# Kernel tuning notes

Measured on AMD Instinct MI355X. Metric: run time of the kernel, lower is better.

The kernel has to match this reference:

```python
import jax, jax.numpy as jnp
import numpy as np

B, L, D, H = 2, 256, 512, 8
DH = D // H
EPS = 1e-12
NEG = -1000000000000000.0


def setup_inputs() -> dict:
    key = jax.random.key(0)
    ks = jax.random.split(key, 16)
    s = 0.02
    return {
        "inputs": jax.random.normal(ks[0], (B, L, D), jnp.float32),
        "pos_embedding": jax.random.normal(ks[1], (B, L, L, D), jnp.float32),
        "seq_mask": jnp.ones((B, L), jnp.int32),
        "Wq": jax.random.normal(ks[2], (D, D), jnp.float32) * s,
        "bq": jnp.zeros((D,), jnp.float32),
        "Wk": jax.random.normal(ks[3], (D, D), jnp.float32) * s,
        "bk": jnp.zeros((D,), jnp.float32),
        "Wv": jax.random.normal(ks[4], (D, D), jnp.float32) * s,
        "bv": jnp.zeros((D,), jnp.float32),
        "Wr": jax.random.normal(ks[5], (D, D), jnp.float32) * s,
        "br": jnp.zeros((D,), jnp.float32),
        "u": jax.random.normal(ks[6], (H, DH), jnp.float32),
        "v": jax.random.normal(ks[7], (H, DH), jnp.float32),
        "Wf": jax.random.normal(ks[8], (D, D), jnp.float32) * s,
        "bf": jnp.zeros((D,), jnp.float32),
        "gamma": jnp.ones((D,), jnp.float32),
        "beta": jnp.zeros((D,), jnp.float32),
    }


def _layer_norm(x, gamma, beta, eps):
    mu = jnp.mean(x, axis=-1, keepdims=True)
    var = jnp.mean(jnp.square(x - mu), axis=-1, keepdims=True)
    return (x - mu) * jax.lax.rsqrt(var + eps) * gamma + beta


def reference(inputs, pos_embedding, seq_mask, Wq, bq, Wk, bk, Wv, bv, Wr, br,
              u, v, Wf, bf, gamma, beta):
    b, l, d = inputs.shape
    # projections (nn.Linear: x @ W.T + b)
    q = (inputs @ Wq.T + bq).reshape(b, l, H, DH).transpose(0, 2, 1, 3)  # [B,H,L,DH]
    k = (inputs @ Wk.T + bk).reshape(b, l, H, DH).transpose(0, 2, 1, 3)
    vv = (inputs @ Wv.T + bv).reshape(b, l, H, DH).transpose(0, 2, 1, 3)
    rel = (pos_embedding @ Wr.T + br).reshape(b, l, l, H, DH)            # [B,L,L,H,DH]

    # A + C: content-content + content-bias
    A_C = jnp.einsum('bhid,bhjd->bhij', q + u[None, :, None, :], k)
    # B + D: position term against per-(i,j) relative embeddings
    B_D = jnp.einsum('bhid,bijhd->bhij', q + v[None, :, None, :], rel)

    score = (A_C + B_D) / np.sqrt(DH).astype(np.float32)
    invalid = (seq_mask == 0)[:, None, None, :]   # mask keys where seq_mask==0
    score = jnp.where(invalid, NEG, score)
    attn = jax.nn.softmax(score, axis=-1)

    ctx = jnp.einsum('bhij,bhjd->bhid', attn, vv)
    ctx = ctx.transpose(0, 2, 1, 3).reshape(b, l, d)

    # FFN (single dense) + residual + LayerNorm
    h = ctx @ Wf.T + bf
    return _layer_norm(h + inputs, gamma, beta, EPS)
```

## Files before the change

kernel.cpp:

```cpp
#include <hip/hip_runtime.h>
#include <cmath>

typedef __bf16 bf16x8 __attribute__((ext_vector_type(8)));
typedef float f32x4 __attribute__((ext_vector_type(4)));

__device__ __forceinline__ float4 ld4(const float* p) { return *reinterpret_cast<const float4*>(p); }
__device__ __forceinline__ void st4(float* p, float4 v) { *reinterpret_cast<float4*>(p) = v; }
__device__ __forceinline__ void fma4(float4& a, float s, const float4& v) {
    a.x = fmaf(s, v.x, a.x); a.y = fmaf(s, v.y, a.y);
    a.z = fmaf(s, v.z, a.z); a.w = fmaf(s, v.w, a.w);
}
__device__ __forceinline__ float dot4(const float4& a, const float4& b) {
    return a.x*b.x + a.y*b.y + a.z*b.z + a.w*b.w;
}
__device__ __forceinline__ unsigned short f2bf(float f) {
    unsigned int x = __float_as_uint(f);
    unsigned int r = x + 0x7FFFu + ((x >> 16) & 1u);
    return (unsigned short)(r >> 16);
}
__device__ __forceinline__ ushort4 cvt4u(float4 a) {
    ushort4 u;
    u.x = f2bf(a.x); u.y = f2bf(a.y); u.z = f2bf(a.z); u.w = f2bf(a.w);
    return u;
}
__device__ __forceinline__ bf16x8 cvt8(float4 a, float4 b) {
    bf16x8 r;
    r[0] = (__bf16)a.x; r[1] = (__bf16)a.y; r[2] = (__bf16)a.z; r[3] = (__bf16)a.w;
    r[4] = (__bf16)b.x; r[5] = (__bf16)b.y; r[6] = (__bf16)b.z; r[7] = (__bf16)b.w;
    return r;
}

__device__ __forceinline__ void mfma_tile(
        const float* __restrict__ Abase, int ldA,
        const float* __restrict__ Bbase, int ldB,
        int K, int lane, f32x4 acc[4]) {
    int koff = (lane >> 4) * 8;
    int rr = lane & 15;
    const float* ap = Abase + rr * ldA + koff;
    const float* bp = Bbase + rr * ldB + koff;
#pragma unroll 2
    for (int k0 = 0; k0 < K; k0 += 32) {
        float4 a0  = ld4(ap + k0),            a1  = ld4(ap + k0 + 4);
        float4 b00 = ld4(bp + k0),            b01 = ld4(bp + k0 + 4);
        float4 b10 = ld4(bp + 16*ldB + k0),   b11 = ld4(bp + 16*ldB + k0 + 4);
        float4 b20 = ld4(bp + 32*ldB + k0),   b21 = ld4(bp + 32*ldB + k0 + 4);
        float4 b30 = ld4(bp + 48*ldB + k0),   b31 = ld4(bp + 48*ldB + k0 + 4);
        bf16x8 af = cvt8(a0, a1);
        acc[0] = __builtin_amdgcn_mfma_f32_16x16x32_bf16(af, cvt8(b00, b01), acc[0], 0, 0, 0);
        acc[1] = __builtin_amdgcn_mfma_f32_16x16x32_bf16(af, cvt8(b10, b11), acc[1], 0, 0, 0);
        acc[2] = __builtin_amdgcn_mfma_f32_16x16x32_bf16(af, cvt8(b20, b21), acc[2], 0, 0, 0);
        acc[3] = __builtin_amdgcn_mfma_f32_16x16x32_bf16(af, cvt8(b30, b31), acc[3], 0, 0, 0);
    }
}

__global__ __launch_bounds__(256) void k_front(
        const float* __restrict__ x,
        const float* __restrict__ Wq, const float* __restrict__ Wk, const float* __restrict__ Wv,
        const float* __restrict__ bq, const float* __restrict__ bk, const float* __restrict__ bv,
        const float* __restrict__ Wr,
        float* __restrict__ qw, float* __restrict__ kw, float* __restrict__ vw,
        float* __restrict__ wrt) {
    int id = blockIdx.x;
    int t = threadIdx.x;
    if (id < 192) {
        int mat = id >> 6, rem = id & 63;
        int m0 = (rem >> 3) * 64, n0 = (rem & 7) * 64;
        const float* W   = (mat == 0) ? Wq : (mat == 1) ? Wk : Wv;
        const float* bias= (mat == 0) ? bq : (mat == 1) ? bk : bv;
        float* out       = (mat == 0) ? qw : (mat == 1) ? kw : vw;
        int wv = t >> 6, lane = t & 63;
        f32x4 acc[4] = {{0,0,0,0},{0,0,0,0},{0,0,0,0},{0,0,0,0}};
        mfma_tile(x + (m0 + wv * 16) * 512, 512, W + n0 * 512, 512, 512, lane, acc);
        int h = n0 >> 6;
        int col = lane & 15, rbase = (lane >> 4) * 4;
#pragma unroll
        for (int c = 0; c < 4; c++) {
            int d = c * 16 + col;
            float bv_ = bias[n0 + d];
#pragma unroll
            for (int r = 0; r < 4; r++) {
                int m = m0 + wv * 16 + rbase + r;
                int b = m >> 8, i = m & 255;
                out[((b * 8 + h) * 256 + i) * 64 + d] = acc[c][r] + bv_;
            }
        }
    } else {
        __shared__ float tile[64][65];
        int id2 = id - 192;
        int n0 = (id2 >> 3) * 64, k0 = (id2 & 7) * 64;
        int tx = t & 63, ty = t >> 6;
#pragma unroll
        for (int r = 0; r < 16; r++) {
            int row = ty * 16 + r;
            tile[row][tx] = Wr[(n0 + row) * 512 + k0 + tx];
        }
        __syncthreads();
#pragma unroll
        for (int r = 0; r < 16; r++) {
            int row = ty * 16 + r;
            wrt[(k0 + row) * 512 + n0 + tx] = tile[tx][row];
        }
    }
}

__global__ __launch_bounds__(256) void k_mid(
        const float* __restrict__ qw, const float* __restrict__ kw,
        const float* __restrict__ wrt,
        const float* __restrict__ u, const float* __restrict__ vb, const float* __restrict__ br,
        float* __restrict__ w_ws, float* __restrict__ ac_ws) {
    int id = blockIdx.x;
    int t = threadIdx.x, wv = t >> 6, lane = t & 63;
    __shared__ float red[8][64];
    if (id < 512) {
        int h = id >> 6, rem = id & 63;
        int m0 = (rem >> 3) * 64, n0 = (rem & 7) * 64;
        int b = m0 >> 8, i0 = m0 & 255;
        {
            int e = t & 63, grp = t >> 6;
            const float* wr_row = wrt + (size_t)(n0 + e) * 512 + h * 64 + grp * 16;
            const float* vbh = vb + h * 64 + grp * 16;
            float s = 0.f;
#pragma unroll
            for (int d = 0; d < 16; d += 4) s += dot4(ld4(wr_row + d), ld4(vbh + d));
            red[grp][e] = s;
        }
        __syncthreads();
        __shared__ float vwr_l[64];
        if (t < 64) vwr_l[t] = red[0][t] + red[1][t] + red[2][t] + red[3][t];
        f32x4 acc[4] = {{0,0,0,0},{0,0,0,0},{0,0,0,0},{0,0,0,0}};
        mfma_tile(qw + ((b * 8 + h) * 256 + i0 + wv * 16) * 64, 64,
                  wrt + (size_t)n0 * 512 + h * 64, 512, 64, lane, acc);
        __syncthreads();
        int col = lane & 15, rbase = (lane >> 4) * 4;
#pragma unroll
        for (int c = 0; c < 4; c++) {
            float vw_ = vwr_l[c * 16 + col];
            int n = n0 + c * 16 + col;
#pragma unroll
            for (int r = 0; r < 4; r++) {
                int m = m0 + wv * 16 + rbase + r;
                w_ws[((size_t)m * 8 + h) * 512 + n] = acc[c][r] + vw_;
            }
        }
    } else {
        int id2 = id - 512;
        int bh = id2 >> 4, rem2 = id2 & 15;
        int b = bh >> 3, h = bh & 7;
        int i0 = (rem2 >> 2) * 64, j0 = (rem2 & 3) * 64;
        {
            int xx = t & 63, grp = t >> 6;
            const float* qrow = qw + ((b * 8 + h) * 256 + i0 + xx) * 64 + grp * 16;
            const float* brh = br + h * 64 + grp * 16;
            const float* vbh = vb + h * 64 + grp * 16;
            float s = 0.f;
#pragma unroll
            for (int d = 0; d < 16; d += 4) {
                float4 q4 = ld4(qrow + d), b4 = ld4(brh + d), v4 = ld4(vbh + d);
                s += (q4.x + v4.x) * b4.x + (q4.y + v4.y) * b4.y
                   + (q4.z + v4.z) * b4.z + (q4.w + v4.w) * b4.w;
            }
            red[grp][xx] = s;
            const float* krow = kw + ((b * 8 + h) * 256 + j0 + xx) * 64 + grp * 16;
            const float* uh = u + h * 64 + grp * 16;
            s = 0.f;
#pragma unroll
            for (int d = 0; d < 16; d += 4) s += dot4(ld4(krow + d), ld4(uh + d));
            red[4 + grp][xx] = s;
        }
        __syncthreads();
        __shared__ float c_l[64], uk_l[64];
        if (t < 64) c_l[t] = red[0][t] + red[1][t] + red[2][t] + red[3][t];
        else if (t < 128) { int y = t - 64; uk_l[y] = red[4][y] + red[5][y] + red[6][y] + red[7][y]; }
        f32x4 acc[4] = {{0,0,0,0},{0,0,0,0},{0,0,0,0},{0,0,0,0}};
        mfma_tile(qw + ((b * 8 + h) * 256 + i0 + wv * 16) * 64, 64,
                  kw + ((b * 8 + h) * 256 + j0) * 64, 64, 64, lane, acc);
        __syncthreads();
        int col = lane & 15, rbase = (lane >> 4) * 4;
#pragma unroll
        for (int c = 0; c < 4; c++) {
            int j = j0 + c * 16 + col;
            float ukv = uk_l[c * 16 + col];
#pragma unroll
            for (int r = 0; r < 4; r++) {
                int ii = wv * 16 + rbase + r;
                ac_ws[((b * 256 + i0 + ii) * 8 + h) * 256 + j] = acc[c][r] + ukv + c_l[ii];
            }
        }
    }
}

__global__ __launch_bounds__(512, 4) void k_attn(
        const float* __restrict__ pos, const float* __restrict__ w_ws,
        const float* __restrict__ ac_ws, const float* __restrict__ vw,
        const int* __restrict__ seq_mask, float* __restrict__ ctx) {
    int bi = blockIdx.x;
    int b = bi >> 8, i = bi & 255;
    int t = threadIdx.x;
    int wv = t >> 6, lane = t & 63;
    __shared__ unsigned short wl[8 * 512];
    __shared__ float sc[8][256];
    __shared__ unsigned short stage[8][4096];

    {
        int h = t >> 6;
        int e0 = (t & 63) * 8;
        const float* src = w_ws + ((size_t)bi * 8 + h) * 512 + e0;
        float4 a = ld4(src);
        float4 c = ld4(src + 4);
        *reinterpret_cast<ushort4*>(&wl[h * 512 + e0])     = cvt4u(a);
        *reinterpret_cast<ushort4*>(&wl[h * 512 + e0 + 4]) = cvt4u(c);
    }
    __syncthreads();

    const float* pb = pos + (size_t)bi * (256 * 512);
    int jbase = wv * 32;
    unsigned short* sb = &stage[wv][0];
    int arow = lane & 15;
    int koff = (lane >> 4) * 8;

#pragma unroll
    for (int jt = 0; jt < 2; jt++) {
        f32x4 acc = {0, 0, 0, 0};
#pragma unroll
        for (int eh = 0; eh < 2; eh++) {
            const float* src = pb + (size_t)(jbase + jt * 16) * 512 + eh * 256 + lane * 4;
            float4 tmp[16];
#pragma unroll
            for (int s = 0; s < 16; s++) tmp[s] = ld4(src + s * 512);
#pragma unroll
            for (int s = 0; s < 16; s++) {
                *reinterpret_cast<ushort4*>(&sb[s * 256 + lane * 4]) = cvt4u(tmp[s]);
            }
#pragma unroll
            for (int es = 0; es < 8; es++) {
                bf16x8 af = *reinterpret_cast<const bf16x8*>(&sb[arow * 256 + es * 32 + koff]);
                bf16x8 bf = *reinterpret_cast<const bf16x8*>(&wl[(lane & 7) * 512 + (eh * 8 + es) * 32 + koff]);
                acc = __builtin_amdgcn_mfma_f32_16x16x32_bf16(af, bf, acc, 0, 0, 0);
            }
        }
        int h = lane & 15;
        int rbase = (lane >> 4) * 4;
        if (h < 8) {
#pragma unroll
            for (int r = 0; r < 4; r++) sc[h][jbase + jt * 16 + rbase + r] = acc[r];
        }
    }
    __syncthreads();

    {
        int h = wv;
        const float* acrow = ac_ws + ((b * 256 + i) * 8 + h) * 256;
        float vals[4];
        float mx = -INFINITY;
#pragma unroll
        for (int r = 0; r < 4; r++) {
            int j = lane + r * 64;
            float s = (sc[h][j] + acrow[j]) * 0.125f;
            if (seq_mask[b * 256 + j] == 0) s = -1e15f;
            vals[r] = s;
            mx = fmaxf(mx, s);
        }
#pragma unroll
        for (int m = 32; m >= 1; m >>= 1) mx = fmaxf(mx, __shfl_xor(mx, m, 64));
        float sum = 0.f;
#pragma unroll
        for (int r = 0; r < 4; r++) { vals[r] = __expf(vals[r] - mx); sum += vals[r]; }
#pragma unroll
        for (int m = 32; m >= 1; m >>= 1) sum += __shfl_xor(sum, m, 64);
        float inv = 1.0f / sum;
#pragma unroll
        for (int r = 0; r < 4; r++) sc[h][lane + r * 64] = vals[r] * inv;
    }

    float4* part = reinterpret_cast<float4*>(&stage[0][0]);
    {
        int h = wv;
        int d4 = (lane & 15) * 4;
        int js = lane >> 4;
        const float* vbase = vw + (size_t)(b * 8 + h) * 256 * 64 + d4;
        float4 acc = {0, 0, 0, 0};
#pragma unroll 2
        for (int r = 0; r < 64; r += 4) {
            int j = js * 64 + r;
            float p0 = sc[h][j + 0], p1 = sc[h][j + 1];
            float p2 = sc[h][j + 2], p3 = sc[h][j + 3];
            float4 v0 = ld4(vbase + (size_t)(j + 0) * 64);
            float4 v1 = ld4(vbase + (size_t)(j + 1) * 64);
            float4 v2 = ld4(vbase + (size_t)(j + 2) * 64);
            float4 v3 = ld4(vbase + (size_t)(j + 3) * 64);
            fma4(acc, p0, v0); fma4(acc, p1, v1);
            fma4(acc, p2, v2); fma4(acc, p3, v3);
        }
        part[(h * 4 + js) * 16 + (lane & 15)] = acc;
    }
    {
        int h = wv;
        if ((lane >> 4) == 0) {
            int l = lane & 15;
            float4 a0 = part[(h * 4 + 0) * 16 + l], a1 = part[(h * 4 + 1) * 16 + l];
            float4 a2 = part[(h * 4 + 2) * 16 + l], a3 = part[(h * 4 + 3) * 16 + l];
            float4 o;
            o.x = a0.x + a1.x + a2.x + a3.x;
            o.y = a0.y + a1.y + a2.y + a3.y;
            o.z = a0.z + a1.z + a2.z + a3.z;
            o.w = a0.w + a1.w + a2.w + a3.w;
            st4(ctx + (size_t)(b * 256 + i) * 512 + h * 64 + l * 4, o);
        }
    }
}

__global__ __launch_bounds__(256) void k_ffn(
        const float* __restrict__ A, const float* __restrict__ Wf,
        const float* __restrict__ bias, const float* __restrict__ resid,
        float* __restrict__ outp) {
    int m0 = blockIdx.x * 64, n0 = blockIdx.y * 64;
    int t = threadIdx.x, wv = t >> 6, lane = t & 63;
    f32x4 acc[4] = {{0,0,0,0},{0,0,0,0},{0,0,0,0},{0,0,0,0}};
    mfma_tile(A + (m0 + wv * 16) * 512, 512, Wf + n0 * 512, 512, 512, lane, acc);
    int col = lane & 15, rbase = (lane >> 4) * 4;
#pragma unroll
    for (int c = 0; c < 4; c++) {
        int n = n0 + c * 16 + col;
        float bv_ = bias[n];
#pragma unroll
        for (int r = 0; r < 4; r++) {
            int m = m0 + wv * 16 + rbase + r;
            outp[m * 512 + n] = acc[c][r] + bv_ + resid[m * 512 + n];
        }
    }
}

__global__ __launch_bounds__(256) void k_ln(
        const float* __restrict__ tmp, const float* __restrict__ gamma,
        const float* __restrict__ beta, float* __restrict__ out) {
    int m = blockIdx.x, t = threadIdx.x;
    int wv = t >> 6, lane = t & 63;
    float2 xv = *reinterpret_cast<const float2*>(&tmp[m * 512 + t * 2]);
    __shared__ float red[4];
    float s = xv.x + xv.y;
#pragma unroll
    for (int k = 32; k >= 1; k >>= 1) s += __shfl_xor(s, k, 64);
    if (lane == 0) red[wv] = s;
    __syncthreads();
    float mu = (red[0] + red[1] + red[2] + red[3]) * (1.0f / 512.0f);
    __syncthreads();
    float dx = xv.x - mu, dy = xv.y - mu;
    float vs = dx * dx + dy * dy;
#pragma unroll
    for (int k = 32; k >= 1; k >>= 1) vs += __shfl_xor(vs, k, 64);
    if (lane == 0) red[wv] = vs;
    __syncthreads();
    float var = (red[0] + red[1] + red[2] + red[3]) * (1.0f / 512.0f);
    float rstd = rsqrtf(var + 1e-12f);
    float2 g = *reinterpret_cast<const float2*>(&gamma[t * 2]);
    float2 be = *reinterpret_cast<const float2*>(&beta[t * 2]);
    float2 o;
    o.x = dx * rstd * g.x + be.x;
    o.y = dy * rstd * g.y + be.y;
    *reinterpret_cast<float2*>(&out[m * 512 + t * 2]) = o;
}

extern "C" void kernel_launch(void* const* d_in, const int* in_sizes, int n_in,
                              void* d_out, int out_size, void* d_ws, size_t ws_size,
                              hipStream_t stream) {
    const float* x     = (const float*)d_in[0];
    const float* pos   = (const float*)d_in[1];
    const int*   smask = (const int*)d_in[2];
    const float* Wq = (const float*)d_in[3];
    const float* bq = (const float*)d_in[4];
    const float* Wk = (const float*)d_in[5];
    const float* bk = (const float*)d_in[6];
    const float* Wv = (const float*)d_in[7];
    const float* bv = (const float*)d_in[8];
    const float* Wr = (const float*)d_in[9];
    const float* br = (const float*)d_in[10];
    const float* u  = (const float*)d_in[11];
    const float* vb = (const float*)d_in[12];
    const float* Wf = (const float*)d_in[13];
    const float* bf = (const float*)d_in[14];
    const float* gamma = (const float*)d_in[15];
    const float* beta  = (const float*)d_in[16];
    float* out = (float*)d_out;

    float* ws = (float*)d_ws;
    float* q_ws   = ws;
    float* k_ws   = q_ws  + 262144;
    float* v_ws   = k_ws  + 262144;
    float* w_ws   = v_ws  + 262144;
    float* ac_ws  = w_ws  + 2097152;
    float* ctx_ws = ac_ws + 1048576;
    float* tmp_ws = ctx_ws + 262144;
    float* wrt_ws = tmp_ws + 262144;

    k_front<<<dim3(256), 256, 0, stream>>>(x, Wq, Wk, Wv, bq, bk, bv, Wr,
                                           q_ws, k_ws, v_ws, wrt_ws);
    k_mid<<<dim3(768), 256, 0, stream>>>(q_ws, k_ws, wrt_ws, u, vb, br, w_ws, ac_ws);
    k_attn<<<dim3(512), 512, 0, stream>>>(pos, w_ws, ac_ws, v_ws, smask, ctx_ws);
    k_ffn<<<dim3(8, 8), 256, 0, stream>>>(ctx_ws, Wf, bf, x, tmp_ws);
    k_ln<<<dim3(512), 256, 0, stream>>>(tmp_ws, gamma, beta, out);
}
```

Before: 110.7 us.

## Fuse FFN GEMM with residual add and LayerNorm into one kernel

Merges the output projection GEMM and the LayerNorm into a single kernel. Each block computes 16 full rows of 512 columns, so row statistics can be reduced in registers and shared memory, and the intermediate tmp buffer write and re-read go away. This also removes one kernel launch. In exchange the grid shrinks from 64 blocks to 32, each doing more serial work with B loaded directly from global memory. Variance now uses the single-pass E[x^2]-mu^2 form, which is slightly less numerically robust.

```diff
diff --git a/kernel.cpp b/kernel.cpp
--- a/kernel.cpp
+++ b/kernel.cpp
@@ -1,5 +1,6 @@
 #include <hip/hip_runtime.h>
 #include <cmath>
+
 
 typedef __bf16 bf16x8 __attribute__((ext_vector_type(8)));
 typedef float f32x4 __attribute__((ext_vector_type(4)));
@@ -309,55 +310,84 @@
     }
 }
 
-__global__ __launch_bounds__(256) void k_ffn(
+__global__ __launch_bounds__(256) void k_out(
         const float* __restrict__ A, const float* __restrict__ Wf,
-        const float* __restrict__ bias, const float* __restrict__ resid,
+        const float* __restrict__ bf, const float* __restrict__ resid,
+        const float* __restrict__ gamma, const float* __restrict__ beta,
         float* __restrict__ outp) {
-    int m0 = blockIdx.x * 64, n0 = blockIdx.y * 64;
+    int m0 = blockIdx.x * 16;
     int t = threadIdx.x, wv = t >> 6, lane = t & 63;
-    f32x4 acc[4] = {{0,0,0,0},{0,0,0,0},{0,0,0,0},{0,0,0,0}};
-    mfma_tile(A + (m0 + wv * 16) * 512, 512, Wf + n0 * 512, 512, 512, lane, acc);
+    int rr = lane & 15, koff = (lane >> 4) * 8;
     int col = lane & 15, rbase = (lane >> 4) * 4;
-#pragma unroll
-    for (int c = 0; c < 4; c++) {
-        int n = n0 + c * 16 + col;
-        float bv_ = bias[n];
+    const float* ap = A + (size_t)(m0 + rr) * 512 + koff;
+    f32x4 acc[8];
+#pragma unroll
+    for (int nt = 0; nt < 8; nt++) acc[nt] = (f32x4){0, 0, 0, 0};
+#pragma unroll 2
+    for (int k0 = 0; k0 < 512; k0 += 32) {
+        float4 a0 = ld4(ap + k0), a1 = ld4(ap + k0 + 4);
+        bf16x8 af = cvt8(a0, a1);
+#pragma unroll
+        for (int nt = 0; nt < 8; nt++) {
+            int n = wv * 128 + nt * 16 + rr;
+            float4 b0 = ld4(&Wf[(size_t)n * 512 + k0 + koff]);
+            float4 b1 = ld4(&Wf[(size_t)n * 512 + k0 + koff + 4]);
+            acc[nt] = __builtin_amdgcn_mfma_f32_16x16x32_bf16(af, cvt8(b0, b1), acc[nt], 0, 0, 0);
+        }
+    }
+    float vals[8][4];
+    float psum[4] = {0, 0, 0, 0}, psq[4] = {0, 0, 0, 0};
+#pragma unroll
+    for (int nt = 0; nt < 8; nt++) {
+        int n = wv * 128 + nt * 16 + col;
+        float bfn = bf[n];
 #pragma unroll
         for (int r = 0; r < 4; r++) {
-            int m = m0 + wv * 16 + rbase + r;
-            outp[m * 512 + n] = acc[c][r] + bv_ + resid[m * 512 + n];
-        }
-    }
-}
-
-__global__ __launch_bounds__(256) void k_ln(
-        const float* __restrict__ tmp, const float* __restrict__ gamma,
-        const float* __restrict__ beta, float* __restrict__ out) {
-    int m = blockIdx.x, t = threadIdx.x;
-    int wv = t >> 6, lane = t & 63;
-    float2 xv = *reinterpret_cast<const float2*>(&tmp[m * 512 + t * 2]);
-    __shared__ float red[4];
-    float s = xv.x + xv.y;
-#pragma unroll
-    for (int k = 32; k >= 1; k >>= 1) s += __shfl_xor(s, k, 64);
-    if (lane == 0) red[wv] = s;
+            int m = m0 + rbase + r;
+            float v = acc[nt][r] + bfn + resid[(size_t)m * 512 + n];
+            vals[nt][r] = v;
+            psum[r] += v;
+            psq[r] += v * v;
+        }
+    }
+#pragma unroll
+    for (int msk = 1; msk < 16; msk <<= 1) {
+#pragma unroll
+        for (int r = 0; r < 4; r++) {
+            psum[r] += __shfl_xor(psum[r], msk, 64);
+            psq[r]  += __shfl_xor(psq[r],  msk, 64);
+        }
+    }
+    __shared__ float redS[16][4], redQ[16][4];
+    if ((lane & 15) == 0) {
+#pragma unroll
+        for (int r = 0; r < 4; r++) {
+            redS[rbase + r][wv] = psum[r];
+            redQ[rbase + r][wv] = psq[r];
+        }
+    }
     __syncthreads();
-    float mu = (red[0] + red[1] + red[2] + red[3]) * (1.0f / 512.0f);
-    __syncthreads();
-    float dx = xv.x - mu, dy = xv.y - mu;
-    float vs = dx * dx + dy * dy;
-#pragma unroll
-    for (int k = 32; k >= 1; k >>= 1) vs += __shfl_xor(vs, k, 64);
-    if (lane == 0) red[wv] = vs;
-    __syncthreads();
-    float var = (red[0] + red[1] + red[2] + red[3]) * (1.0f / 512.0f);
-    float rstd = rsqrtf(var + 1e-12f);
-    float2 g = *reinterpret_cast<const float2*>(&gamma[t * 2]);
-    float2 be = *reinterpret_cast<const float2*>(&beta[t * 2]);
-    float2 o;
-    o.x = dx * rstd * g.x + be.x;
-    o.y = dy * rstd * g.y + be.y;
-    *reinterpret_cast<float2*>(&out[m * 512 + t * 2]) = o;
+    float mu[4], rstd[4];
+#pragma unroll
+    for (int r = 0; r < 4; r++) {
+        int row = rbase + r;
+        float s = redS[row][0] + redS[row][1] + redS[row][2] + redS[row][3];
+        float q = redQ[row][0] + redQ[row][1] + redQ[row][2] + redQ[row][3];
+        float m_ = s * (1.0f / 512.0f);
+        float var = q * (1.0f / 512.0f) - m_ * m_;
+        mu[r] = m_;
+        rstd[r] = rsqrtf(var + 1e-12f);
+    }
+#pragma unroll
+    for (int nt = 0; nt < 8; nt++) {
+        int n = wv * 128 + nt * 16 + col;
+        float g = gamma[n], be = beta[n];
+#pragma unroll
+        for (int r = 0; r < 4; r++) {
+            int m = m0 + rbase + r;
+            outp[(size_t)m * 512 + n] = (vals[nt][r] - mu[r]) * rstd[r] * g + be;
+        }
+    }
 }
 
 extern "C" void kernel_launch(void* const* d_in, const int* in_sizes, int n_in,
@@ -389,13 +419,11 @@
     float* w_ws   = v_ws  + 262144;
     float* ac_ws  = w_ws  + 2097152;
     float* ctx_ws = ac_ws + 1048576;
-    float* tmp_ws = ctx_ws + 262144;
-    float* wrt_ws = tmp_ws + 262144;
+    float* wrt_ws = ctx_ws + 262144;
 
     k_front<<<dim3(256), 256, 0, stream>>>(x, Wq, Wk, Wv, bq, bk, bv, Wr,
                                            q_ws, k_ws, v_ws, wrt_ws);
     k_mid<<<dim3(768), 256, 0, stream>>>(q_ws, k_ws, wrt_ws, u, vb, br, w_ws, ac_ws);
     k_attn<<<dim3(512), 512, 0, stream>>>(pos, w_ws, ac_ws, v_ws, smask, ctx_ws);
-    k_ffn<<<dim3(8, 8), 256, 0, stream>>>(ctx_ws, Wf, bf, x, tmp_ws);
-    k_ln<<<dim3(512), 256, 0, stream>>>(tmp_ws, gamma, beta, out);
-}
+    k_out<<<dim3(32), 256, 0, stream>>>(ctx_ws, Wf, bf, x, gamma, beta, out);
+}
```

After: 141.7 us. 1.28x slower.
